# Performance work log

Hardware: AMD Instinct MI355X
Metric: run time of the kernel (lower is better)

The kernel has to match this reference:

```python
import jax, jax.numpy as jnp
import numpy as np

B, S, D, H, HD, MLP = 2, 4096, 512, 8, 64, 2048
BLK, C = 128, 32  # Fixed1Pattern(block_size=128), Fixed2Pattern(block_size=128, c=32)
EPS = 1e-6


def _xavier(key, shape, fan_in, fan_out):
    lim = np.sqrt(6.0 / (fan_in + fan_out)).astype(np.float32)
    return jax.random.uniform(key, shape, jnp.float32, -lim, lim)


def setup_inputs() -> dict:
    key = jax.random.key(0)
    ks = jax.random.split(key, 9)
    return {
        "inputs": jax.random.normal(ks[0], (B, S, D), jnp.float32),
        "ln1_scale": jnp.ones((D,), jnp.float32),
        "ln1_bias": jnp.zeros((D,), jnp.float32),
        "wq": _xavier(ks[1], (D, H, HD), D, H * HD),
        "wk": _xavier(ks[2], (D, H, HD), D, H * HD),
        "wv": _xavier(ks[3], (D, H, HD), D, H * HD),
        "wo": _xavier(ks[4], (H, HD, D), H * HD, D),
        "ln2_scale": jnp.ones((D,), jnp.float32),
        "ln2_bias": jnp.zeros((D,), jnp.float32),
        "w1": _xavier(ks[5], (D, MLP), D, MLP),
        "b1": jax.random.normal(ks[6], (MLP,), jnp.float32) * 1e-6,
        "w2": _xavier(ks[7], (MLP, D), MLP, D),
        "b2": jax.random.normal(ks[8], (D,), jnp.float32) * 1e-6,
    }


def _layer_norm(x, scale, bias):
    mu = jnp.mean(x, axis=-1, keepdims=True)
    var = jnp.mean(jnp.square(x - mu), axis=-1, keepdims=True)
    return (x - mu) * jax.lax.rsqrt(var + EPS) * scale + bias


def _sparse_mask():
    # Union of causal Fixed1 (same block) and Fixed2 (last C columns of each block) patterns.
    i = jnp.arange(S)[:, None]
    j = jnp.arange(S)[None, :]
    causal = j <= i
    local = (i // BLK) == (j // BLK)            # Fixed1: within-block
    strided = (j % BLK) >= (BLK - C)            # Fixed2: block-summary columns
    return causal & (local | strided)           # [S, S] bool


def reference(inputs, ln1_scale, ln1_bias, wq, wk, wv, wo,
              ln2_scale, ln2_bias, w1, b1, w2, b2):
    x = _layer_norm(inputs, ln1_scale, ln1_bias)
    q = jnp.einsum("bsd,dhk->bshk", x, wq)
    k = jnp.einsum("bsd,dhk->bshk", x, wk)
    v = jnp.einsum("bsd,dhk->bshk", x, wv)
    scale = 1.0 / np.sqrt(HD).astype(np.float32)
    scores = jnp.einsum("bqhk,bshk->bhqs", q * scale, k)  # [B,H,S,S]
    mask = _sparse_mask()[None, None]
    scores = jnp.where(mask, scores, jnp.float32(-1e9))
    attn = jax.nn.softmax(scores, axis=-1)
    ctx = jnp.einsum("bhqs,bshk->bqhk", attn, v)
    attn_out = jnp.einsum("bqhk,hkd->bqd", ctx, wo)
    x = attn_out + inputs  # residual 1 (dropout deterministic)
    y = _layer_norm(x, ln2_scale, ln2_bias)
    y = jax.nn.gelu(y @ w1 + b1) @ w2 + b2  # MlpBlock
    return x + y
```

## Files before the change

kernel.cpp:

```cpp
#include <hip/hip_runtime.h>
#include <hip/hip_bf16.h>

typedef __attribute__((ext_vector_type(8))) __bf16 bf16x8;
typedef __attribute__((ext_vector_type(8))) short s16x8;
typedef __attribute__((ext_vector_type(4))) float f32x4;

#define NB 2
#define NS 4096
#define ND 512
#define NH 8
#define NHD 64
#define NMLP 2048

__device__ __forceinline__ unsigned short f2b(float f) {
  __hip_bfloat16 h = __float2bfloat16(f);
  return __builtin_bit_cast(unsigned short, h);
}

__device__ __forceinline__ float geluf(float x) {
  return 0.5f * x * (1.0f + tanhf(0.7978845608028654f * (x + 0.044715f * x * x * x)));
}

__device__ __forceinline__ void gload16(const void* g, void* l) {
  __builtin_amdgcn_global_load_lds((const __attribute__((address_space(1))) void*)g,
                                   (__attribute__((address_space(3))) void*)l, 16, 0, 0);
}

__global__ __launch_bounds__(256) void prep_weights(const float* __restrict__ wq,
                                                    const float* __restrict__ wk,
                                                    const float* __restrict__ wv,
                                                    const float* __restrict__ wo,
                                                    const float* __restrict__ w1,
                                                    const float* __restrict__ w2,
                                                    unsigned short* __restrict__ qkvT,
                                                    unsigned short* __restrict__ woT,
                                                    unsigned short* __restrict__ w1T,
                                                    unsigned short* __restrict__ w2T) {
  __shared__ unsigned short lt[64][66];
  const int tile = blockIdx.x, t = threadIdx.x;
  const float* src;
  unsigned short* dst;
  int R, C, tr, tc;
  float sc = 1.0f;
  if (tile < 256) {
    int seg = tile >> 6, tt = tile & 63;
    R = 512; C = 512;
    src = seg == 0 ? wq : seg == 1 ? wk : seg == 2 ? wv : wo;
    dst = (seg < 3) ? (qkvT + ((size_t)seg << 18)) : woT;
    if (seg == 0) sc = 0.125f;
    tr = tt >> 3; tc = tt & 7;
  } else if (tile < 512) {
    int tt = tile - 256;
    R = 512; C = 2048; src = w1; dst = w1T;
    tr = tt >> 5; tc = tt & 31;
  } else {
    int tt = tile - 512;
    R = 2048; C = 512; src = w2; dst = w2T;
    tr = tt >> 3; tc = tt & 7;
  }
  const int r0 = tr * 64, c0 = tc * 64;
  const int fx = t & 15, fy = t >> 4;
#pragma unroll
  for (int p = 0; p < 4; ++p) {
    int rr = p * 16 + fy;
    float4 v = *(const float4*)&src[(size_t)(r0 + rr) * C + c0 + fx * 4];
    lt[rr][fx * 4 + 0] = f2b(v.x * sc);
    lt[rr][fx * 4 + 1] = f2b(v.y * sc);
    lt[rr][fx * 4 + 2] = f2b(v.z * sc);
    lt[rr][fx * 4 + 3] = f2b(v.w * sc);
  }
  __syncthreads();
#pragma unroll
  for (int p = 0; p < 4; ++p) {
    int cc = p * 16 + fy;
    ushort4 o;
    o.x = lt[fx * 4 + 0][cc];
    o.y = lt[fx * 4 + 1][cc];
    o.z = lt[fx * 4 + 2][cc];
    o.w = lt[fx * 4 + 3][cc];
    *(ushort4*)&dst[(size_t)(c0 + cc) * R + r0 + fx * 4] = o;
  }
}

__global__ __launch_bounds__(256) void ln_bf16(const float* __restrict__ x,
                                               const float* __restrict__ g,
                                               const float* __restrict__ bta,
                                               unsigned short* __restrict__ out) {
  const int t = threadIdx.x, l = t & 63, w = t >> 6;
  const size_t row = (size_t)blockIdx.x * 4 + w;
  const float4* xr = (const float4*)(x + row * ND);
  float4 a = xr[l];
  float4 bq = xr[64 + l];
  float s = a.x + a.y + a.z + a.w + bq.x + bq.y + bq.z + bq.w;
  float ss = a.x * a.x + a.y * a.y + a.z * a.z + a.w * a.w +
             bq.x * bq.x + bq.y * bq.y + bq.z * bq.z + bq.w * bq.w;
#pragma unroll
  for (int msk = 1; msk <= 32; msk <<= 1) {
    s += __shfl_xor(s, msk);
    ss += __shfl_xor(ss, msk);
  }
  float mu = s * (1.0f / ND);
  float var = ss * (1.0f / ND) - mu * mu;
  float rr = rsqrtf(var + 1e-6f);
  const float4* g4 = (const float4*)g;
  const float4* b4 = (const float4*)bta;
  float4 g0 = g4[l], g1 = g4[64 + l], b0 = b4[l], b1 = b4[64 + l];
  ushort4 o0, o1;
  o0.x = f2b((a.x - mu) * rr * g0.x + b0.x);
  o0.y = f2b((a.y - mu) * rr * g0.y + b0.y);
  o0.z = f2b((a.z - mu) * rr * g0.z + b0.z);
  o0.w = f2b((a.w - mu) * rr * g0.w + b0.w);
  o1.x = f2b((bq.x - mu) * rr * g1.x + b1.x);
  o1.y = f2b((bq.y - mu) * rr * g1.y + b1.y);
  o1.z = f2b((bq.z - mu) * rr * g1.z + b1.z);
  o1.w = f2b((bq.w - mu) * rr * g1.w + b1.w);
  ushort4* orow = (ushort4*)(out + row * ND);
  orow[l] = o0;
  orow[64 + l] = o1;
}

template <int EPI>
__global__ __launch_bounds__(256) void gemm_bt(const unsigned short* __restrict__ A,
                                               const unsigned short* __restrict__ Bt,
                                               int M, int N, int K,
                                               unsigned short* __restrict__ ob,
                                               float* __restrict__ of,
                                               const float* __restrict__ addf,
                                               const float* __restrict__ bias) {
  __shared__ unsigned short lA[2][128 * 64];
  __shared__ unsigned short lB[2][128 * 64];
  const int t = threadIdx.x;
  const int l = t & 63, w = t >> 6;
  const int wr = w >> 1, wc = w & 1;
  const int gx = gridDim.x;
  const int nwg = gx * gridDim.y;
  const int fid = blockIdx.y * gx + blockIdx.x;
  const int q8 = nwg >> 3, r8 = nwg & 7, xcd = fid & 7, idx = fid >> 3;
  const int lid = (xcd < r8 ? xcd * (q8 + 1) : r8 * (q8 + 1) + (xcd - r8) * q8) + idx;
  const int bm = lid / gx, bn = lid % gx;
  const size_t rowBytes = (size_t)K * 2;
  const char* Ab = (const char*)A + (size_t)bm * 128 * rowBytes;
  const char* Bb = (const char*)Bt + (size_t)bn * 128 * rowBytes;
  const int srow0 = t >> 3;
  const int scb = (((t & 7) ^ ((t >> 3) & 7)) << 4);
  f32x4 acc[4][4] = {};

  auto stage = [&](int buf, int k0) {
    char* dA = (char*)&lA[buf][0] + t * 16;
    char* dB = (char*)&lB[buf][0] + t * 16;
#pragma unroll
    for (int i = 0; i < 4; ++i) {
      const size_t go = (size_t)(srow0 + i * 32) * rowBytes + 2 * k0 + scb;
      gload16(Ab + go, dA + i * 4096);
      gload16(Bb + go, dB + i * 4096);
    }
  };

  const int nkt = K >> 6;
  stage(0, 0);
  int cur = 0;
  for (int kt = 0; kt < nkt; ++kt) {
    if (kt + 1 < nkt) {
      stage(cur ^ 1, (kt + 1) * 64);
      asm volatile("s_waitcnt vmcnt(8)" ::: "memory");
    } else {
      asm volatile("s_waitcnt vmcnt(0)" ::: "memory");
    }
    __builtin_amdgcn_s_barrier();
    __builtin_amdgcn_sched_barrier(0);
#pragma unroll
    for (int ks = 0; ks < 2; ++ks) {
      const int xg = ((ks * 4 + (l >> 4)) ^ (l & 7)) * 8;
      bf16x8 aF[4], bF[4];
#pragma unroll
      for (int m = 0; m < 4; ++m)
        aF[m] = *(const bf16x8*)&lA[cur][(wr * 64 + m * 16 + (l & 15)) * 64 + xg];
#pragma unroll
      for (int n = 0; n < 4; ++n)
        bF[n] = *(const bf16x8*)&lB[cur][(wc * 64 + n * 16 + (l & 15)) * 64 + xg];
      __builtin_amdgcn_s_setprio(1);
#pragma unroll
      for (int m = 0; m < 4; ++m)
#pragma unroll
        for (int n = 0; n < 4; ++n)
          acc[m][n] = __builtin_amdgcn_mfma_f32_16x16x32_bf16(aF[m], bF[n], acc[m][n], 0, 0, 0);
      __builtin_amdgcn_s_setprio(0);
    }
    asm volatile("s_waitcnt lgkmcnt(0)" ::: "memory");
    __builtin_amdgcn_s_barrier();
    cur ^= 1;
  }
#pragma unroll
  for (int m = 0; m < 4; ++m)
#pragma unroll
    for (int n = 0; n < 4; ++n) {
      int row0 = bm * 128 + wr * 64 + m * 16 + (l >> 4) * 4;
      int col = bn * 128 + wc * 64 + n * 16 + (l & 15);
      if constexpr (EPI == 0) {
        int part = col >> 9, nn = col & 511;
        int hh = nn >> 6, hd = nn & 63;
        int b = row0 >> 12, sidx0 = row0 & 4095;
        if (part < 2) {
#pragma unroll
          for (int j = 0; j < 4; ++j)
            ob[((((size_t)part * NB + b) * NH + hh) * NS + sidx0 + j) * NHD + hd] =
                f2b(acc[m][n][j]);
        } else {
          ushort4 o;
          o.x = f2b(acc[m][n][0]);
          o.y = f2b(acc[m][n][1]);
          o.z = f2b(acc[m][n][2]);
          o.w = f2b(acc[m][n][3]);
          *(ushort4*)&ob[(size_t)2 * NB * NH * NS * NHD +
                         (((size_t)b * NH + hh) * NHD + hd) * NS + sidx0] = o;
        }
      } else {
#pragma unroll
        for (int j = 0; j < 4; ++j) {
          int row = row0 + j;
          float v = acc[m][n][j];
          if constexpr (EPI == 1) {
            size_t i = (size_t)row * ND + col;
            of[i] = v + addf[i];
          } else if constexpr (EPI == 2) {
            size_t i = (size_t)row * NMLP + col;
            ob[i] = f2b(geluf(v + bias[col]));
          } else if constexpr (EPI == 3) {
            size_t i = (size_t)row * ND + col;
            of[i] = v + bias[col] + addf[i];
          }
        }
      }
    }
}

__global__ __launch_bounds__(512, 4) void attn_sparse(const unsigned short* __restrict__ qm,
                                                      const unsigned short* __restrict__ km,
                                                      const unsigned short* __restrict__ vTg,
                                                      unsigned short* __restrict__ ctx) {
  __shared__ unsigned short kl[128 * 72];
  __shared__ unsigned short vt[64 * 136];
  __shared__ unsigned short pl[8][16 * 72];
  const int t = threadIdx.x, l = t & 63, w = t >> 6;
  const int bid = blockIdx.x;
  const int qbRaw = bid & 31, hh = (bid >> 5) & 7, b = bid >> 8;
  const int qb = b ? (31 - qbRaw) : qbRaw;
  const size_t bh = ((size_t)b * NH + hh) * NS;
  const size_t bhd = ((size_t)b * NH + hh) * NHD;
  const int qrow0 = qb * 128 + w * 16;
  bf16x8 qa[2];
#pragma unroll
  for (int ks = 0; ks < 2; ++ks)
    qa[ks] = *(const bf16x8*)&qm[(bh + qrow0 + (l & 15)) * NHD + ks * 32 + (l >> 4) * 8];
  f32x4 c[4] = {};
  float mrun[4], lrun[4];
#pragma unroll
  for (int j = 0; j < 4; ++j) { mrun[j] = -1e30f; lrun[j] = 0.0f; }

  const int nsum128 = qb >> 2, rem = qb & 3;
  const int nSumCh = nsum128 + (rem ? 1 : 0);
  const int nch = nSumCh + 1;
  const int kkey = t >> 2, kd = (t & 3) * 16;
  const int vd = t >> 3, vk = (t & 7) * 16;

  s16x8 kr0, kr1, vr0, vr1;
  auto issueLoads = [&](int c2) {
    int grK, sV;
    if (c2 < nSumCh) {
      grK = ((c2 << 2) + (kkey >> 5)) * 128 + 96 + (kkey & 31);
      sV = ((c2 << 2) + (vk >> 5)) * 128 + 96 + (vk & 31);
    } else {
      grK = qb * 128 + kkey;
      sV = qb * 128 + vk;
    }
    const unsigned short* kp = &km[(bh + grK) * NHD + kd];
    kr0 = *(const s16x8*)kp;
    kr1 = *(const s16x8*)(kp + 8);
    const unsigned short* vp = &vTg[(bhd + vd) * NS + sV];
    vr0 = *(const s16x8*)vp;
    vr1 = *(const s16x8*)(vp + 8);
  };

  issueLoads(0);
  for (int ch = 0; ch < nch; ++ch) {
    if (ch) {
      asm volatile("s_waitcnt lgkmcnt(0)" ::: "memory");
      __builtin_amdgcn_s_barrier();
    }
    *(s16x8*)&kl[kkey * 72 + kd] = kr0;
    *(s16x8*)&kl[kkey * 72 + kd + 8] = kr1;
    *(s16x8*)&vt[vd * 136 + vk] = vr0;
    *(s16x8*)&vt[vd * 136 + vk + 8] = vr1;
    asm volatile("s_waitcnt lgkmcnt(0)" ::: "memory");
    __builtin_amdgcn_s_barrier();
    __builtin_amdgcn_sched_barrier(0);
    if (ch + 1 < nch) issueLoads(ch + 1);

    const bool isLocal = (ch == nch - 1);
    const bool isRem = (rem != 0) && !isLocal && (ch == nsum128);
    const int nT = isLocal ? (w + 1) : (isRem ? 2 * rem : 8);
    const int nTpl = isLocal ? ((w | 1) + 1) : nT;
    const int nKs = nTpl >> 1;

    f32x4 sf[8];
#pragma unroll
    for (int n = 0; n < 8; ++n) {
      if (n < nT) {
        const bf16x8 k0 = *(const bf16x8*)&kl[(n * 16 + (l & 15)) * 72 + (l >> 4) * 8];
        const bf16x8 k1 = *(const bf16x8*)&kl[(n * 16 + (l & 15)) * 72 + 32 + (l >> 4) * 8];
        f32x4 a = {};
        a = __builtin_amdgcn_mfma_f32_16x16x32_bf16(qa[0], k0, a, 0, 0, 0);
        a = __builtin_amdgcn_mfma_f32_16x16x32_bf16(qa[1], k1, a, 0, 0, 0);
        if (isLocal && n == w) {
#pragma unroll
          for (int j = 0; j < 4; ++j)
            if ((l & 15) > (l >> 4) * 4 + j) a[j] = -1e9f;
        }
        sf[n] = a;
      }
    }
    float cm[4], al[4];
#pragma unroll
    for (int j = 0; j < 4; ++j) cm[j] = -1e30f;
#pragma unroll
    for (int n = 0; n < 8; ++n)
      if (n < nT)
#pragma unroll
        for (int j = 0; j < 4; ++j) cm[j] = fmaxf(cm[j], sf[n][j]);
#pragma unroll
    for (int j = 0; j < 4; ++j) {
      cm[j] = fmaxf(cm[j], __shfl_xor(cm[j], 1));
      cm[j] = fmaxf(cm[j], __shfl_xor(cm[j], 2));
      cm[j] = fmaxf(cm[j], __shfl_xor(cm[j], 4));
      cm[j] = fmaxf(cm[j], __shfl_xor(cm[j], 8));
      float nm = fmaxf(mrun[j], cm[j]);
      al[j] = __expf(mrun[j] - nm);
      mrun[j] = nm;
    }
#pragma unroll
    for (int n = 0; n < 4; ++n)
#pragma unroll
      for (int j = 0; j < 4; ++j) c[n][j] *= al[j];
    float rs[4] = {0.f, 0.f, 0.f, 0.f};
#pragma unroll
    for (int n = 0; n < 8; ++n)
      if (n < nT)
#pragma unroll
        for (int j = 0; j < 4; ++j) {
          float p = __expf(sf[n][j] - mrun[j]);
          sf[n][j] = p;
          rs[j] += p;
        }
#pragma unroll
    for (int j = 0; j < 4; ++j) {
      rs[j] += __shfl_xor(rs[j], 1);
      rs[j] += __shfl_xor(rs[j], 2);
      rs[j] += __shfl_xor(rs[j], 4);
      rs[j] += __shfl_xor(rs[j], 8);
      lrun[j] = lrun[j] * al[j] + rs[j];
    }
#pragma unroll
    for (int h = 0; h < 2; ++h) {
      if (h * 4 < nTpl) {
#pragma unroll
        for (int n2 = 0; n2 < 4; ++n2) {
          const int n = h * 4 + n2;
#pragma unroll
          for (int j = 0; j < 4; ++j) {
            if (n < nTpl) {
              unsigned short pv = 0;
              if (n < nT) pv = f2b(sf[n][j]);
              pl[w][((l >> 4) * 4 + j) * 72 + n2 * 16 + (l & 15)] = pv;
            }
          }
        }
#pragma unroll
        for (int ks2 = 0; ks2 < 2; ++ks2) {
          const int ks = h * 2 + ks2;
          if (ks < nKs) {
            const bf16x8 pa = *(const bf16x8*)&pl[w][(l & 15) * 72 + ks2 * 32 + (l >> 4) * 8];
#pragma unroll
            for (int nd = 0; nd < 4; ++nd) {
              const bf16x8 vb =
                  *(const bf16x8*)&vt[(nd * 16 + (l & 15)) * 136 + ks * 32 + (l >> 4) * 8];
              c[nd] = __builtin_amdgcn_mfma_f32_16x16x32_bf16(pa, vb, c[nd], 0, 0, 0);
            }
          }
        }
      }
    }
  }
#pragma unroll
  for (int n = 0; n < 4; ++n)
#pragma unroll
    for (int j = 0; j < 4; ++j) {
      int srow = qrow0 + (l >> 4) * 4 + j;
      int col = n * 16 + (l & 15);
      ctx[((size_t)b * NS + srow) * ND + hh * NHD + col] = f2b(c[n][j] / lrun[j]);
    }
}

extern "C" void kernel_launch(void* const* d_in, const int* in_sizes, int n_in,
                              void* d_out, int out_size, void* d_ws, size_t ws_size,
                              hipStream_t stream) {
  (void)in_sizes; (void)n_in; (void)out_size; (void)ws_size;
  const float* inputs = (const float*)d_in[0];
  const float* ln1s = (const float*)d_in[1];
  const float* ln1b = (const float*)d_in[2];
  const float* wq = (const float*)d_in[3];
  const float* wk = (const float*)d_in[4];
  const float* wv = (const float*)d_in[5];
  const float* wo = (const float*)d_in[6];
  const float* ln2s = (const float*)d_in[7];
  const float* ln2b = (const float*)d_in[8];
  const float* w1 = (const float*)d_in[9];
  const float* b1 = (const float*)d_in[10];
  const float* w2 = (const float*)d_in[11];
  const float* b2 = (const float*)d_in[12];
  float* out = (float*)d_out;

  unsigned short* xln = (unsigned short*)d_ws;
  unsigned short* xln2 = xln + (size_t)8192 * 512;
  unsigned short* ctx = xln2 + (size_t)8192 * 512;
  unsigned short* qkv = ctx + (size_t)8192 * 512;
  float* xres = (float*)(qkv + (size_t)3 * 8192 * 512);
  unsigned short* hbuf = (unsigned short*)(xres + (size_t)8192 * 512);
  unsigned short* qkvT = hbuf + (size_t)8192 * 2048;
  unsigned short* woT = qkvT + (size_t)1536 * 512;
  unsigned short* w1T = woT + (size_t)512 * 512;
  unsigned short* w2T = w1T + (size_t)2048 * 512;

  prep_weights<<<768, 256, 0, stream>>>(wq, wk, wv, wo, w1, w2, qkvT, woT, w1T, w2T);
  ln_bf16<<<2048, 256, 0, stream>>>(inputs, ln1s, ln1b, xln);
  gemm_bt<0><<<dim3(12, 64), 256, 0, stream>>>(xln, qkvT, 8192, 1536, 512,
                                               qkv, nullptr, nullptr, nullptr);
  attn_sparse<<<512, 512, 0, stream>>>(qkv, qkv + (size_t)8192 * 512,
                                       qkv + (size_t)2 * 8192 * 512, ctx);
  gemm_bt<1><<<dim3(4, 64), 256, 0, stream>>>(ctx, woT, 8192, 512, 512,
                                              nullptr, xres, inputs, nullptr);
  ln_bf16<<<2048, 256, 0, stream>>>(xres, ln2s, ln2b, xln2);
  gemm_bt<2><<<dim3(16, 64), 256, 0, stream>>>(xln2, w1T, 8192, 2048, 512,
                                               hbuf, nullptr, nullptr, b1);
  gemm_bt<3><<<dim3(4, 64), 256, 0, stream>>>(hbuf, w2T, 8192, 512, 2048,
                                              nullptr, out, xres, b2);
}
```

Before: 172.3 us.

## Use 8-wave GEMM tiles, lazy softmax rescale, exp-based GELU, reordered attention grid

The GEMM kernel moves from 4 to 8 waves per 128x128 tile, so each wave holds a 64x32 accumulator and issues half as many loads per stage. The aim is more latency hiding and lower register pressure. Attention now rescales its running max only when the new block max exceeds the old by more than 8, which skips most exp and multiply work but lets accumulators grow larger. It also interleaves heads across the block index for load balance and multiplies by a reciprocal instead of dividing. GELU replaces tanhf with an algebraically equivalent form built on __expf.

```diff
diff --git a/kernel.cpp b/kernel.cpp
--- a/kernel.cpp
+++ b/kernel.cpp
@@ -18,7 +18,8 @@
 }
 
 __device__ __forceinline__ float geluf(float x) {
-  return 0.5f * x * (1.0f + tanhf(0.7978845608028654f * (x + 0.044715f * x * x * x)));
+  float u = 0.7978845608028654f * (x + 0.044715f * x * x * x);
+  return x / (1.0f + __expf(-2.0f * u));
 }
 
 __device__ __forceinline__ void gload16(const void* g, void* l) {
@@ -120,7 +121,7 @@
 }
 
 template <int EPI>
-__global__ __launch_bounds__(256) void gemm_bt(const unsigned short* __restrict__ A,
+__global__ __launch_bounds__(512) void gemm_bt(const unsigned short* __restrict__ A,
                                                const unsigned short* __restrict__ Bt,
                                                int M, int N, int K,
                                                unsigned short* __restrict__ ob,
@@ -131,7 +132,7 @@
   __shared__ unsigned short lB[2][128 * 64];
   const int t = threadIdx.x;
   const int l = t & 63, w = t >> 6;
-  const int wr = w >> 1, wc = w & 1;
+  const int wr = w >> 2, wc = w & 3;
   const int gx = gridDim.x;
   const int nwg = gx * gridDim.y;
   const int fid = blockIdx.y * gx + blockIdx.x;
@@ -141,18 +142,18 @@
   const size_t rowBytes = (size_t)K * 2;
   const char* Ab = (const char*)A + (size_t)bm * 128 * rowBytes;
   const char* Bb = (const char*)Bt + (size_t)bn * 128 * rowBytes;
-  const int srow0 = t >> 3;
+  const int sr0 = t >> 3;
   const int scb = (((t & 7) ^ ((t >> 3) & 7)) << 4);
-  f32x4 acc[4][4] = {};
+  f32x4 acc[4][2] = {};
 
   auto stage = [&](int buf, int k0) {
     char* dA = (char*)&lA[buf][0] + t * 16;
     char* dB = (char*)&lB[buf][0] + t * 16;
 #pragma unroll
-    for (int i = 0; i < 4; ++i) {
-      const size_t go = (size_t)(srow0 + i * 32) * rowBytes + 2 * k0 + scb;
-      gload16(Ab + go, dA + i * 4096);
-      gload16(Bb + go, dB + i * 4096);
+    for (int i = 0; i < 2; ++i) {
+      const size_t go = (size_t)(sr0 + i * 64) * rowBytes + 2 * k0 + scb;
+      gload16(Ab + go, dA + i * 8192);
+      gload16(Bb + go, dB + i * 8192);
     }
   };
 
@@ -162,7 +163,7 @@
   for (int kt = 0; kt < nkt; ++kt) {
     if (kt + 1 < nkt) {
       stage(cur ^ 1, (kt + 1) * 64);
-      asm volatile("s_waitcnt vmcnt(8)" ::: "memory");
+      asm volatile("s_waitcnt vmcnt(4)" ::: "memory");
     } else {
       asm volatile("s_waitcnt vmcnt(0)" ::: "memory");
     }
@@ -171,18 +172,18 @@
 #pragma unroll
     for (int ks = 0; ks < 2; ++ks) {
       const int xg = ((ks * 4 + (l >> 4)) ^ (l & 7)) * 8;
-      bf16x8 aF[4], bF[4];
+      bf16x8 aF[4], bF[2];
 #pragma unroll
       for (int m = 0; m < 4; ++m)
         aF[m] = *(const bf16x8*)&lA[cur][(wr * 64 + m * 16 + (l & 15)) * 64 + xg];
 #pragma unroll
-      for (int n = 0; n < 4; ++n)
-        bF[n] = *(const bf16x8*)&lB[cur][(wc * 64 + n * 16 + (l & 15)) * 64 + xg];
+      for (int n = 0; n < 2; ++n)
+        bF[n] = *(const bf16x8*)&lB[cur][(wc * 32 + n * 16 + (l & 15)) * 64 + xg];
       __builtin_amdgcn_s_setprio(1);
 #pragma unroll
       for (int m = 0; m < 4; ++m)
 #pragma unroll
-        for (int n = 0; n < 4; ++n)
+        for (int n = 0; n < 2; ++n)
           acc[m][n] = __builtin_amdgcn_mfma_f32_16x16x32_bf16(aF[m], bF[n], acc[m][n], 0, 0, 0);
       __builtin_amdgcn_s_setprio(0);
     }
@@ -193,9 +194,9 @@
 #pragma unroll
   for (int m = 0; m < 4; ++m)
 #pragma unroll
-    for (int n = 0; n < 4; ++n) {
+    for (int n = 0; n < 2; ++n) {
       int row0 = bm * 128 + wr * 64 + m * 16 + (l >> 4) * 4;
-      int col = bn * 128 + wc * 64 + n * 16 + (l & 15);
+      int col = bn * 128 + wc * 32 + n * 16 + (l & 15);
       if constexpr (EPI == 0) {
         int part = col >> 9, nn = col & 511;
         int hh = nn >> 6, hd = nn & 63;
@@ -214,6 +215,12 @@
           *(ushort4*)&ob[(size_t)2 * NB * NH * NS * NHD +
                          (((size_t)b * NH + hh) * NHD + hd) * NS + sidx0] = o;
         }
+      } else if constexpr (EPI == 2) {
+#pragma unroll
+        for (int j = 0; j < 4; ++j) {
+          size_t i = (size_t)(row0 + j) * NMLP + col;
+          ob[i] = f2b(geluf(acc[m][n][j] + bias[col]));
+        }
       } else {
 #pragma unroll
         for (int j = 0; j < 4; ++j) {
@@ -222,10 +229,7 @@
           if constexpr (EPI == 1) {
             size_t i = (size_t)row * ND + col;
             of[i] = v + addf[i];
-          } else if constexpr (EPI == 2) {
-            size_t i = (size_t)row * NMLP + col;
-            ob[i] = f2b(geluf(v + bias[col]));
-          } else if constexpr (EPI == 3) {
+          } else {
             size_t i = (size_t)row * ND + col;
             of[i] = v + bias[col] + addf[i];
           }
@@ -243,8 +247,10 @@
   __shared__ unsigned short pl[8][16 * 72];
   const int t = threadIdx.x, l = t & 63, w = t >> 6;
   const int bid = blockIdx.x;
-  const int qbRaw = bid & 31, hh = (bid >> 5) & 7, b = bid >> 8;
-  const int qb = b ? (31 - qbRaw) : qbRaw;
+  const int hh = bid & 7;
+  const int jj = bid >> 3;
+  const int b = jj >> 5;
+  const int qb = (jj < 32) ? jj : 63 - jj;
   const size_t bh = ((size_t)b * NH + hh) * NS;
   const size_t bhd = ((size_t)b * NH + hh) * NHD;
   const int qrow0 = qb * 128 + w * 16;
@@ -319,7 +325,7 @@
         sf[n] = a;
       }
     }
-    float cm[4], al[4];
+    float cm[4];
 #pragma unroll
     for (int j = 0; j < 4; ++j) cm[j] = -1e30f;
 #pragma unroll
@@ -333,14 +339,25 @@
       cm[j] = fmaxf(cm[j], __shfl_xor(cm[j], 2));
       cm[j] = fmaxf(cm[j], __shfl_xor(cm[j], 4));
       cm[j] = fmaxf(cm[j], __shfl_xor(cm[j], 8));
-      float nm = fmaxf(mrun[j], cm[j]);
-      al[j] = __expf(mrun[j] - nm);
-      mrun[j] = nm;
-    }
-#pragma unroll
-    for (int n = 0; n < 4; ++n)
-#pragma unroll
-      for (int j = 0; j < 4; ++j) c[n][j] *= al[j];
+    }
+    bool need = false;
+#pragma unroll
+    for (int j = 0; j < 4; ++j) need |= (cm[j] > mrun[j] + 8.0f);
+    if (__any(need)) {
+      float al[4];
+#pragma unroll
+      for (int j = 0; j < 4; ++j) {
+        float nm = fmaxf(mrun[j], cm[j]);
+        al[j] = __expf(mrun[j] - nm);
+        mrun[j] = nm;
+      }
+#pragma unroll
+      for (int n = 0; n < 4; ++n)
+#pragma unroll
+        for (int j = 0; j < 4; ++j) c[n][j] *= al[j];
+#pragma unroll
+      for (int j = 0; j < 4; ++j) lrun[j] *= al[j];
+    }
     float rs[4] = {0.f, 0.f, 0.f, 0.f};
 #pragma unroll
     for (int n = 0; n < 8; ++n)
@@ -357,7 +374,7 @@
       rs[j] += __shfl_xor(rs[j], 2);
       rs[j] += __shfl_xor(rs[j], 4);
       rs[j] += __shfl_xor(rs[j], 8);
-      lrun[j] = lrun[j] * al[j] + rs[j];
+      lrun[j] += rs[j];
     }
 #pragma unroll
     for (int h = 0; h < 2; ++h) {
@@ -390,13 +407,16 @@
       }
     }
   }
+  float rinv[4];
+#pragma unroll
+  for (int j = 0; j < 4; ++j) rinv[j] = 1.0f / lrun[j];
 #pragma unroll
   for (int n = 0; n < 4; ++n)
 #pragma unroll
     for (int j = 0; j < 4; ++j) {
       int srow = qrow0 + (l >> 4) * 4 + j;
       int col = n * 16 + (l & 15);
-      ctx[((size_t)b * NS + srow) * ND + hh * NHD + col] = f2b(c[n][j] / lrun[j]);
+      ctx[((size_t)b * NS + srow) * ND + hh * NHD + col] = f2b(c[n][j] * rinv[j]);
     }
 }
 
@@ -432,15 +452,15 @@
 
   prep_weights<<<768, 256, 0, stream>>>(wq, wk, wv, wo, w1, w2, qkvT, woT, w1T, w2T);
   ln_bf16<<<2048, 256, 0, stream>>>(inputs, ln1s, ln1b, xln);
-  gemm_bt<0><<<dim3(12, 64), 256, 0, stream>>>(xln, qkvT, 8192, 1536, 512,
+  gemm_bt<0><<<dim3(12, 64), 512, 0, stream>>>(xln, qkvT, 8192, 1536, 512,
                                                qkv, nullptr, nullptr, nullptr);
   attn_sparse<<<512, 512, 0, stream>>>(qkv, qkv + (size_t)8192 * 512,
                                        qkv + (size_t)2 * 8192 * 512, ctx);
-  gemm_bt<1><<<dim3(4, 64), 256, 0, stream>>>(ctx, woT, 8192, 512, 512,
+  gemm_bt<1><<<dim3(4, 64), 512, 0, stream>>>(ctx, woT, 8192, 512, 512,
                                               nullptr, xres, inputs, nullptr);
   ln_bf16<<<2048, 256, 0, stream>>>(xres, ln2s, ln2b, xln2);
-  gemm_bt<2><<<dim3(16, 64), 256, 0, stream>>>(xln2, w1T, 8192, 2048, 512,
+  gemm_bt<2><<<dim3(16, 64), 512, 0, stream>>>(xln2, w1T, 8192, 2048, 512,
                                                hbuf, nullptr, nullptr, b1);
-  gemm_bt<3><<<dim3(4, 64), 256, 0, stream>>>(hbuf, w2T, 8192, 512, 2048,
+  gemm_bt<3><<<dim3(4, 64), 512, 0, stream>>>(hbuf, w2T, 8192, 512, 2048,
                                               nullptr, out, xres, b2);
 }
```

After: 158.4 us. 1.09x faster.
